# Kernel optimization log

Measured on AMD Instinct MI355X. Metric: run time of the kernel, lower is better.

The kernel has to match this reference:

```python
import jax, jax.numpy as jnp
import numpy as np

D_MODEL = 1024
D_STATE = 16
D_CONV = 4
EXPAND = 2
D_INNER = EXPAND * D_MODEL
DT_RANK = (D_MODEL + 15) // 16  # 64
EPS = 1e-5


def dwconv(x, w, b, pad):
    # x: (B, C, L), w: (C, 1, K), depthwise conv
    y = jax.lax.conv_general_dilated(x, w, (1,), [pad],
                                     dimension_numbers=('NCH', 'OIH', 'NCH'),
                                     feature_group_count=x.shape[1])
    return y + b[None, :, None]


def mamba(x, W_inproj, m_conv_w, m_conv_b, W_xproj, W_dt, b_dt, A_log, Dp, W_outproj):
    # x: (B, L, d_model)
    Bn, L, _ = x.shape
    xz = x @ W_inproj.T                       # (B, L, 2*d_inner)
    xi, z = jnp.split(xz, 2, axis=-1)
    # causal depthwise conv: pad (K-1, 0) == torch pad K-1 then slice [:L]
    xc = dwconv(jnp.swapaxes(xi, 1, 2), m_conv_w, m_conv_b, (D_CONV - 1, 0))
    u = jax.nn.silu(jnp.swapaxes(xc, 1, 2))   # (B, L, d_inner)
    x_dbl = u @ W_xproj.T                     # (B, L, dt_rank + 2*d_state)
    dt = x_dbl[..., :DT_RANK]
    Bm = x_dbl[..., DT_RANK:DT_RANK + D_STATE]
    Cm = x_dbl[..., DT_RANK + D_STATE:]
    dt = jax.nn.softplus(dt @ W_dt.T + b_dt)  # (B, L, d_inner)
    A = -jnp.exp(A_log)                       # (d_inner, d_state)

    def step(h, inp):
        dt_t, B_t, C_t, u_t = inp             # (B,di),(B,ds),(B,ds),(B,di)
        dA = jnp.exp(dt_t[..., None] * A)     # (B, di, ds)
        h = dA * h + dt_t[..., None] * B_t[:, None, :] * u_t[..., None]
        y = jnp.einsum('bds,bs->bd', h, C_t)
        return h, y

    tm = lambda a: jnp.swapaxes(a, 0, 1)      # time-major for scan
    h0 = jnp.zeros((Bn, D_INNER, D_STATE), x.dtype)
    _, ys = jax.lax.scan(step, h0, (tm(dt), tm(Bm), tm(Cm), tm(u)))
    y = jnp.swapaxes(ys, 0, 1) + u * Dp       # (B, L, d_inner)
    y = y * jax.nn.silu(z)
    return y @ W_outproj.T                    # (B, L, d_model)


def forward(x, ln_g, ln_b, W_in, b_in, conv_w, conv_b,
            W_inproj, m_conv_w, m_conv_b, W_xproj, W_dt, b_dt,
            A_log, Dp, W_outproj, W_out, b_out):
    h = jnp.swapaxes(x, 1, 2)                 # (B, L, d_model)
    mu = h.mean(-1, keepdims=True)
    var = ((h - mu) ** 2).mean(-1, keepdims=True)
    h = (h - mu) / jnp.sqrt(var + EPS) * ln_g + ln_b
    h = h @ W_in.T + b_in
    # outer depthwise conv: kernel 4, pad 2 each side -> length L+1 (faithful)
    h = dwconv(jnp.swapaxes(h, 1, 2), conv_w, conv_b, (D_CONV // 2, D_CONV // 2))
    h = jax.nn.silu(h)
    h = jnp.swapaxes(h, 1, 2)                 # (B, L+1, d_model)
    y = mamba(h, W_inproj, m_conv_w, m_conv_b, W_xproj, W_dt, b_dt, A_log, Dp, W_outproj)
    y = y @ W_out.T + b_out
    return jnp.swapaxes(y, 1, 2)              # (B, d_model, L+1)


def setup_inputs() -> dict:
    key = jax.random.key(0)
    ks = jax.random.split(key, 16)
    B, L = 2, 2048
    s = 0.02
    inp = {
        'x': jax.random.normal(ks[0], (B, D_MODEL, L), jnp.float32),
        'ln_g': jnp.ones((D_MODEL,), jnp.float32),
        'ln_b': jnp.zeros((D_MODEL,), jnp.float32),
        'W_in': jax.random.normal(ks[1], (D_MODEL, D_MODEL), jnp.float32) * s,
        'b_in': jnp.zeros((D_MODEL,), jnp.float32),
        'conv_w': jax.random.normal(ks[2], (D_MODEL, 1, D_CONV), jnp.float32) * 0.3,
        'conv_b': jnp.zeros((D_MODEL,), jnp.float32),
        'W_inproj': jax.random.normal(ks[3], (2 * D_INNER, D_MODEL), jnp.float32) * s,
        'm_conv_w': jax.random.normal(ks[4], (D_INNER, 1, D_CONV), jnp.float32) * 0.3,
        'm_conv_b': jnp.zeros((D_INNER,), jnp.float32),
        'W_xproj': jax.random.normal(ks[5], (DT_RANK + 2 * D_STATE, D_INNER), jnp.float32) * s,
        'W_dt': jax.random.normal(ks[6], (D_INNER, DT_RANK), jnp.float32) * (DT_RANK ** -0.5),
        'b_dt': jax.random.uniform(ks[7], (D_INNER,), jnp.float32, -4.6, -2.0),
        'A_log': jnp.log(jnp.tile(jnp.arange(1, D_STATE + 1, dtype=jnp.float32)[None, :], (D_INNER, 1))),
        'Dp': jnp.ones((D_INNER,), jnp.float32),
        'W_outproj': jax.random.normal(ks[8], (D_MODEL, D_INNER), jnp.float32) * s,
        'W_out': jax.random.normal(ks[9], (D_MODEL, D_MODEL), jnp.float32) * s,
        'b_out': jnp.zeros((D_MODEL,), jnp.float32),
    }
    return inp


def reference(x, ln_g, ln_b, W_in, b_in, conv_w, conv_b, W_inproj, m_conv_w, m_conv_b,
              W_xproj, W_dt, b_dt, A_log, Dp, W_outproj, W_out, b_out):
    return forward(x, ln_g, ln_b, W_in, b_in, conv_w, conv_b, W_inproj, m_conv_w,
                   m_conv_b, W_xproj, W_dt, b_dt, A_log, Dp, W_outproj, W_out, b_out)
```

## Files before the change

### kernel.cpp

```cpp
#include <hip/hip_runtime.h>
#include <hip/hip_bf16.h>

#define DMODEL 1024
#define DINNER 2048
#define DTRANK 64
#define NPROJ  96
#define BATCH  2
#define LIN    2048
#define LOUT   2049
#define MTOT0  4096
#define MTOT1  4098
#define TC     64
#define NCH    33

typedef __attribute__((ext_vector_type(8))) short short8;
typedef __attribute__((ext_vector_type(4))) float f32x4;

__device__ __forceinline__ float f_silu(float x)     { return x / (1.f + __expf(-x)); }
__device__ __forceinline__ float f_softplus(float x) { return (x > 20.f) ? x : log1pf(__expf(x)); }
__device__ __forceinline__ short f2b(float x)
{
    __hip_bfloat16 b = __float2bfloat16(x);
    return *reinterpret_cast<short*>(&b);
}
__device__ __forceinline__ float b2f(short s)
{
    return __uint_as_float(((unsigned)(unsigned short)s) << 16);
}
__device__ __forceinline__ void gload16(const void* g, void* l)
{
    __builtin_amdgcn_global_load_lds(
        (const __attribute__((address_space(1))) void*)g,
        (__attribute__((address_space(3))) void*)l,
        16, 0, 0);
}

__global__ void ln_stats_k(const float* __restrict__ x, float* __restrict__ mu, float* __restrict__ rs)
{
    int b  = blockIdx.y;
    int l0 = blockIdx.x * 64;
    int lc = threadIdx.x & 63;
    int q  = threadIdx.x >> 6;
    const float* xb = x + (size_t)b * DMODEL * LIN + (l0 + lc);
    float s = 0.f, ss = 0.f;
    for (int c = q * 256; c < q * 256 + 256; ++c) {
        float v = xb[(size_t)c * LIN];
        s += v; ss += v * v;
    }
    __shared__ float Ss[4][64];
    __shared__ float Sq[4][64];
    Ss[q][lc] = s; Sq[q][lc] = ss;
    __syncthreads();
    if (threadIdx.x < 64) {
        float st = Ss[0][lc] + Ss[1][lc] + Ss[2][lc] + Ss[3][lc];
        float sq = Sq[0][lc] + Sq[1][lc] + Sq[2][lc] + Sq[3][lc];
        float m = st * (1.f / DMODEL);
        float v = sq * (1.f / DMODEL) - m * m;
        mu[b * LIN + l0 + lc] = m;
        rs[b * LIN + l0 + lc] = 1.f / sqrtf(v + 1e-5f);
    }
}

__global__ void lnT_k(const float* __restrict__ x, const float* __restrict__ mu,
                      const float* __restrict__ rs, const float* __restrict__ g,
                      const float* __restrict__ be, short* __restrict__ h0T)
{
    __shared__ float T[32][33];
    int l0 = blockIdx.x * 32;
    int c0 = blockIdx.y * 32;
    int b  = blockIdx.z;
    int tx = threadIdx.x & 31, ty = threadIdx.x >> 5;
    const float* xb = x + ((size_t)b * DMODEL + c0) * LIN + l0;
#pragma unroll
    for (int i = 0; i < 4; i++) {
        int cl = ty + 8 * i;
        T[cl][tx] = xb[(size_t)cl * LIN + tx];
    }
    __syncthreads();
    int c = c0 + tx;
    float gg = g[c], bb = be[c];
#pragma unroll
    for (int i = 0; i < 4; i++) {
        int ll = ty + 8 * i;
        int m = b * LIN + l0 + ll;
        float v = (T[tx][ll] - mu[m]) * rs[m] * gg + bb;
        h0T[(size_t)m * DMODEL + c] = f2b(v);
    }
}

__global__ void wdtT_k(const float* __restrict__ W_dt, float* __restrict__ WdtT)
{
    __shared__ float T[32][33];
    int n0 = blockIdx.x * 32;
    int k0 = blockIdx.y * 32;
    int tx = threadIdx.x & 31, ty = threadIdx.x >> 5;
#pragma unroll
    for (int i = 0; i < 4; i++) {
        int r = ty + 8 * i;
        T[r][tx] = W_dt[(size_t)(n0 + r) * 64 + k0 + tx];
    }
    __syncthreads();
#pragma unroll
    for (int i = 0; i < 4; i++) {
        int r = ty + 8 * i;
        WdtT[(size_t)(k0 + r) * 2048 + n0 + tx] = T[tx][r];
    }
}

__global__ void cvt_all_k(const float* __restrict__ W_in, const float* __restrict__ W_inproj,
                          const float* __restrict__ W_xproj, const float* __restrict__ W_dt,
                          const float* __restrict__ W_outproj, const float* __restrict__ W_out,
                          short* __restrict__ Wib, short* __restrict__ Winpb,
                          short* __restrict__ Wxpb, short* __restrict__ Wdtb,
                          short* __restrict__ Wopb, short* __restrict__ Wob)
{
    int b = blockIdx.x;
    const float* s; short* d; int i;
    if      (b < 1024) { s = W_in;      d = Wib;   i = b; }
    else if (b < 5120) { s = W_inproj;  d = Winpb; i = b - 1024; }
    else if (b < 5312) { s = W_xproj;   d = Wxpb;  i = b - 5120; }
    else if (b < 5440) { s = W_dt;      d = Wdtb;  i = b - 5312; }
    else if (b < 7488) { s = W_outproj; d = Wopb;  i = b - 5440; }
    else               { s = W_out;     d = Wob;   i = b - 7488; }
    int idx = (i * 256 + threadIdx.x) * 4;
    float4 v = *(const float4*)(s + idx);
    d[idx + 0] = f2b(v.x); d[idx + 1] = f2b(v.y);
    d[idx + 2] = f2b(v.z); d[idx + 3] = f2b(v.w);
}

template<int EPI>
__global__ __launch_bounds__(256) void gemm_bf(
    const short* __restrict__ A, int lda,
    const short* __restrict__ W, int ldb,
    float* __restrict__ C, int ldc,
    short* __restrict__ Cb, int ldcb,
    int M, int N, int K,
    const float* __restrict__ bias)
{
    __shared__ short As[128 * 32];
    __shared__ short Bs[128 * 32];
    int tid  = threadIdx.x;
    int lane = tid & 63, wid = tid >> 6;
    int wr = wid >> 1, wc = wid & 1;
    int fr = lane & 15, kg = lane >> 4;
    int m0 = blockIdx.x * 128, n0 = blockIdx.y * 128;

    int scol  = (lane & 3) * 8;
    int srow0 = wid * 32 + (lane >> 2);
    int srow1 = srow0 + 16;
    const short* a0 = A + (size_t)(m0 + srow0) * lda + scol;
    const short* a1 = A + (size_t)(m0 + srow1) * lda + scol;
    const short* b0 = W + (size_t)(n0 + srow0) * ldb + scol;
    const short* b1 = W + (size_t)(n0 + srow1) * ldb + scol;
    char* asd0 = (char*)As + (wid * 2 + 0) * 1024;
    char* asd1 = (char*)As + (wid * 2 + 1) * 1024;
    char* bsd0 = (char*)Bs + (wid * 2 + 0) * 1024;
    char* bsd1 = (char*)Bs + (wid * 2 + 1) * 1024;

    f32x4 acc[4][4];
#pragma unroll
    for (int mi = 0; mi < 4; mi++)
#pragma unroll
        for (int ni = 0; ni < 4; ni++) acc[mi][ni] = (f32x4){0.f, 0.f, 0.f, 0.f};

    for (int k0 = 0; k0 < K; k0 += 32) {
        gload16(a0 + k0, asd0);
        gload16(a1 + k0, asd1);
        gload16(b0 + k0, bsd0);
        gload16(b1 + k0, bsd1);
        __syncthreads();

        short8 af[4], bf[4];
#pragma unroll
        for (int mi = 0; mi < 4; mi++)
            af[mi] = *(const short8*)&As[(wr * 64 + mi * 16 + fr) * 32 + kg * 8];
#pragma unroll
        for (int ni = 0; ni < 4; ni++)
            bf[ni] = *(const short8*)&Bs[(wc * 64 + ni * 16 + fr) * 32 + kg * 8];
#pragma unroll
        for (int mi = 0; mi < 4; mi++)
#pragma unroll
            for (int ni = 0; ni < 4; ni++)
                acc[mi][ni] = __builtin_amdgcn_mfma_f32_16x16x32_bf16(
                    af[mi], bf[ni], acc[mi][ni], 0, 0, 0);
        __syncthreads();
    }

#pragma unroll
    for (int ni = 0; ni < 4; ni++) {
        int n = n0 + wc * 64 + ni * 16 + fr;
        if (n >= N) continue;
        float bv = 0.f;
        if (EPI == 1) bv = bias[n];
#pragma unroll
        for (int mi = 0; mi < 4; mi++) {
#pragma unroll
            for (int r = 0; r < 4; r++) {
                int m = m0 + wr * 64 + mi * 16 + kg * 4 + r;
                if (m >= M) continue;
                float v = acc[mi][ni][r];
                if (EPI == 1) v += bv;
                if (EPI == 5) {
                    float vb = v + bias[m];
                    int bq = (n >= LOUT) ? 1 : 0;
                    int l  = n - bq * LOUT;
                    C[((size_t)bq * DMODEL + m) * LOUT + l] = vb;
                } else if (EPI == 4) {
                    Cb[(size_t)m * ldcb + n] = f2b(v);
                } else {
                    C[(size_t)m * ldc + n] = v;
                }
            }
        }
    }
}

__global__ __launch_bounds__(256) void dtfuse2_k(const float* __restrict__ xdbl,
                                                 const float* __restrict__ WdtT,
                                                 const float* __restrict__ b_dt,
                                                 float* __restrict__ dtout)
{
    int t  = threadIdx.x;
    int m0 = blockIdx.x * 8;
    __shared__ float dr[8][64];
    {
        int k = t & 63, r = t >> 6;
        int ma = m0 + r, mb = m0 + r + 4;
        dr[r][k]     = (ma < MTOT1) ? xdbl[(size_t)ma * NPROJ + k] : 0.f;
        dr[r + 4][k] = (mb < MTOT1) ? xdbl[(size_t)mb * NPROJ + k] : 0.f;
    }
    __syncthreads();

    int n0 = t * 4;
    f32x4 acc0[8], acc1[8];
#pragma unroll
    for (int mi = 0; mi < 8; mi++) {
        acc0[mi] = (f32x4){0.f, 0.f, 0.f, 0.f};
        acc1[mi] = (f32x4){0.f, 0.f, 0.f, 0.f};
    }

    for (int k = 0; k < 64; k += 4) {
        f32x4 w0[4], w1[4];
#pragma unroll
        for (int e = 0; e < 4; e++) {
            w0[e] = *(const f32x4*)&WdtT[(size_t)(k + e) * 2048 + n0];
            w1[e] = *(const f32x4*)&WdtT[(size_t)(k + e) * 2048 + n0 + 1024];
        }
#pragma unroll
        for (int mi = 0; mi < 8; mi++) {
            f32x4 d = *(const f32x4*)&dr[mi][k];
#pragma unroll
            for (int e = 0; e < 4; e++) {
                acc0[mi] += d[e] * w0[e];
                acc1[mi] += d[e] * w1[e];
            }
        }
    }

    f32x4 b0 = *(const f32x4*)&b_dt[n0];
    f32x4 b1 = *(const f32x4*)&b_dt[n0 + 1024];
#pragma unroll
    for (int mi = 0; mi < 8; mi++) {
        int m = m0 + mi;
        if (m >= MTOT1) continue;
        f32x4 v0, v1;
#pragma unroll
        for (int e = 0; e < 4; e++) {
            v0[e] = f_softplus(acc0[mi][e] + b0[e]);
            v1[e] = f_softplus(acc1[mi][e] + b1[e]);
        }
        *(f32x4*)&dtout[(size_t)m * DINNER + n0]        = v0;
        *(f32x4*)&dtout[(size_t)m * DINNER + n0 + 1024] = v1;
    }
}

__global__ void conv1_k(const float* __restrict__ h1, const float* __restrict__ cw,
                        const float* __restrict__ cb, short* __restrict__ h2b)
{
    int c = blockIdx.x * 256 + threadIdx.x;
    int m = blockIdx.y;
    int b = (m >= LOUT) ? 1 : 0;
    int l = m - b * LOUT;
    float4 wv = ((const float4*)cw)[c];
    const float* w = (const float*)&wv;
    float acc = cb[c];
#pragma unroll
    for (int k = 0; k < 4; k++) {
        int li = l - 2 + k;
        if (li >= 0 && li < LIN)
            acc += h1[((size_t)b * LIN + li) * DMODEL + c] * w[k];
    }
    h2b[(size_t)m * DMODEL + c] = f2b(f_silu(acc));
}

__global__ void conv2_k(const float* __restrict__ xz, const float* __restrict__ cw,
                        const float* __restrict__ cb, float* __restrict__ u,
                        short* __restrict__ ub)
{
    int d = blockIdx.x * 256 + threadIdx.x;
    int m = blockIdx.y;
    int b = (m >= LOUT) ? 1 : 0;
    int l = m - b * LOUT;
    float4 wv = ((const float4*)cw)[d];
    const float* w = (const float*)&wv;
    float acc = cb[d];
#pragma unroll
    for (int k = 0; k < 4; k++) {
        int li = l - 3 + k;
        if (li >= 0)
            acc += xz[((size_t)b * LOUT + li) * (2 * DINNER) + d] * w[k];
    }
    float s = f_silu(acc);
    u [(size_t)m * DINNER + d] = s;
    ub[(size_t)m * DINNER + d] = f2b(s);
}

__global__ void scan1_k(const float* __restrict__ dt, const float* __restrict__ u,
                        const float* __restrict__ xdbl, const float* __restrict__ A_log,
                        float* __restrict__ sP, float* __restrict__ sH)
{
    int d = blockIdx.x * 256 + threadIdx.x;
    int c = blockIdx.y;
    int b = blockIdx.z;
    int t0 = c * TC;
    int tlen = LOUT - t0; if (tlen > TC) tlen = TC;

    float Ad[16], h[16], P[16];
#pragma unroll
    for (int q = 0; q < 4; q++) {
        float4 av = ((const float4*)A_log)[d * 4 + q];
        Ad[q*4+0] = -__expf(av.x); Ad[q*4+1] = -__expf(av.y);
        Ad[q*4+2] = -__expf(av.z); Ad[q*4+3] = -__expf(av.w);
    }
#pragma unroll
    for (int s = 0; s < 16; s++) { h[s] = 0.f; P[s] = 1.f; }

    size_t row0 = (size_t)b * LOUT + t0;
    const float* dtp = dt + row0 * DINNER + d;
    const float* up  = u  + row0 * DINNER + d;
    const float* Bp  = xdbl + row0 * NPROJ + DTRANK;
    for (int t = 0; t < tlen; t++) {
        float dtt = dtp[(size_t)t * DINNER];
        float du  = dtt * up[(size_t)t * DINNER];
        const float* Bt = Bp + (size_t)t * NPROJ;
#pragma unroll
        for (int s = 0; s < 16; s++) {
            float a = __expf(dtt * Ad[s]);
            h[s] = a * h[s] + du * Bt[s];
            P[s] *= a;
        }
    }
    size_t base = ((size_t)(b * NCH + c) * 16) * DINNER + d;
#pragma unroll
    for (int s = 0; s < 16; s++) {
        sP[base + (size_t)s * DINNER] = P[s];
        sH[base + (size_t)s * DINNER] = h[s];
    }
}

__global__ void scan2_k(const float* __restrict__ sP, float* __restrict__ sH)
{
    int gid = blockIdx.x * 256 + threadIdx.x;
    int d = gid & (DINNER - 1);
    int s = (gid >> 11) & 15;
    int b = gid >> 15;
    size_t base = ((size_t)(b * NCH) * 16 + s) * DINNER + d;
    const size_t cstep = (size_t)16 * DINNER;
    float hrun = 0.f;
    for (int c = 0; c < NCH; c++) {
        size_t idx = base + (size_t)c * cstep;
        float Pv = sP[idx], hl = sH[idx];
        sH[idx] = hrun;
        hrun = Pv * hrun + hl;
    }
}

__global__ void scan3_k(const float* __restrict__ dt, const float* __restrict__ u,
                        const float* __restrict__ xdbl, const float* __restrict__ A_log,
                        const float* __restrict__ Dp, const float* __restrict__ xz,
                        const float* __restrict__ sH, short* __restrict__ ymb)
{
    int d = blockIdx.x * 256 + threadIdx.x;
    int c = blockIdx.y;
    int b = blockIdx.z;
    int t0 = c * TC;
    int tlen = LOUT - t0; if (tlen > TC) tlen = TC;

    float Ad[16], h[16];
#pragma unroll
    for (int q = 0; q < 4; q++) {
        float4 av = ((const float4*)A_log)[d * 4 + q];
        Ad[q*4+0] = -__expf(av.x); Ad[q*4+1] = -__expf(av.y);
        Ad[q*4+2] = -__expf(av.z); Ad[q*4+3] = -__expf(av.w);
    }
    size_t sbase = ((size_t)(b * NCH + c) * 16) * DINNER + d;
#pragma unroll
    for (int s = 0; s < 16; s++) h[s] = sH[sbase + (size_t)s * DINNER];

    float Dpd = Dp[d];
    size_t row0 = (size_t)b * LOUT + t0;
    const float* dtp = dt + row0 * DINNER + d;
    const float* up  = u  + row0 * DINNER + d;
    const float* Bp  = xdbl + row0 * NPROJ + DTRANK;
    const float* Cp  = Bp + 16;
    const float* zp  = xz + row0 * (2 * DINNER) + DINNER + d;
    short* yp = ymb + row0 * DINNER + d;
    for (int t = 0; t < tlen; t++) {
        float dtt = dtp[(size_t)t * DINNER];
        float ut  = up[(size_t)t * DINNER];
        float du  = dtt * ut;
        const float* Bt = Bp + (size_t)t * NPROJ;
        const float* Ct = Cp + (size_t)t * NPROJ;
        float y = 0.f;
#pragma unroll
        for (int s = 0; s < 16; s++) {
            float a = __expf(dtt * Ad[s]);
            h[s] = a * h[s] + du * Bt[s];
            y += h[s] * Ct[s];
        }
        float z = zp[(size_t)t * (2 * DINNER)];
        yp[(size_t)t * DINNER] = f2b((y + ut * Dpd) * f_silu(z));
    }
}

extern "C" void kernel_launch(void* const* d_in, const int* in_sizes, int n_in,
                              void* d_out, int out_size, void* d_ws, size_t ws_size,
                              hipStream_t stream)
{
    (void)in_sizes; (void)n_in; (void)out_size; (void)ws_size;
    const float* x        = (const float*)d_in[0];
    const float* ln_g     = (const float*)d_in[1];
    const float* ln_b     = (const float*)d_in[2];
    const float* W_in     = (const float*)d_in[3];
    const float* b_in     = (const float*)d_in[4];
    const float* conv_w   = (const float*)d_in[5];
    const float* conv_b   = (const float*)d_in[6];
    const float* W_inproj = (const float*)d_in[7];
    const float* m_conv_w = (const float*)d_in[8];
    const float* m_conv_b = (const float*)d_in[9];
    const float* W_xproj  = (const float*)d_in[10];
    const float* W_dt     = (const float*)d_in[11];
    const float* b_dt     = (const float*)d_in[12];
    const float* A_log    = (const float*)d_in[13];
    const float* Dp       = (const float*)d_in[14];
    const float* W_outproj= (const float*)d_in[15];
    const float* W_out    = (const float*)d_in[16];
    const float* b_out    = (const float*)d_in[17];
    float* out = (float*)d_out;

    float* F    = (float*)d_ws;
    float* mu   = F;
    float* rs   = F + 4096;
    float* h1   = F + 8192;
    float* xz   = h1 + (size_t)MTOT0 * DMODEL;
    float* uu   = xz + (size_t)MTOT1 * 2 * DINNER;
    float* xdbl = uu + (size_t)MTOT1 * DINNER;
    float* dt   = xdbl + (size_t)MTOT1 * NPROJ;
    float* sP   = dt + (size_t)MTOT1 * DINNER;
    float* sH   = sP + (size_t)BATCH * NCH * 16 * DINNER;
    float* WdtT = sH + (size_t)BATCH * NCH * 16 * DINNER;
    float* fend = WdtT + (size_t)DTRANK * DINNER;

    short* S     = (short*)fend;
    short* h0T   = S;
    short* h2b   = h0T + (size_t)MTOT0 * DMODEL;
    short* ub    = h2b + (size_t)MTOT1 * DMODEL;
    short* Wib   = ub  + (size_t)MTOT1 * DINNER;
    short* Winpb = Wib   + (size_t)DMODEL * DMODEL;
    short* Wxpb  = Winpb + (size_t)(2*DINNER) * DMODEL;
    short* Wdtb  = Wxpb  + (size_t)NPROJ * DINNER;
    short* Wopb  = Wdtb  + (size_t)DINNER * DTRANK;
    short* Wob   = Wopb  + (size_t)DMODEL * DINNER;
    short* ymb   = ub;
    short* o1b   = (short*)h1;

    cvt_all_k<<<8512, 256, 0, stream>>>(W_in, W_inproj, W_xproj, W_dt, W_outproj, W_out,
                                        Wib, Winpb, Wxpb, Wdtb, Wopb, Wob);
    wdtT_k<<<dim3(64, 2), 256, 0, stream>>>(W_dt, WdtT);
    ln_stats_k<<<dim3(32, 2), 256, 0, stream>>>(x, mu, rs);
    lnT_k<<<dim3(64, 32, 2), 256, 0, stream>>>(x, mu, rs, ln_g, ln_b, h0T);
    gemm_bf<1><<<dim3(32, 8), 256, 0, stream>>>(h0T, DMODEL, Wib, DMODEL,
        h1, DMODEL, nullptr, 0, MTOT0, DMODEL, DMODEL, b_in);
    conv1_k<<<dim3(4, MTOT1), 256, 0, stream>>>(h1, conv_w, conv_b, h2b);
    gemm_bf<0><<<dim3(33, 32), 256, 0, stream>>>(h2b, DMODEL, Winpb, DMODEL,
        xz, 2 * DINNER, nullptr, 0, MTOT1, 2 * DINNER, DMODEL, nullptr);
    conv2_k<<<dim3(8, MTOT1), 256, 0, stream>>>(xz, m_conv_w, m_conv_b, uu, ub);
    gemm_bf<0><<<dim3(33, 1), 256, 0, stream>>>(ub, DINNER, Wxpb, DINNER,
        xdbl, NPROJ, nullptr, 0, MTOT1, NPROJ, DINNER, nullptr);
    dtfuse2_k<<<513, 256, 0, stream>>>(xdbl, WdtT, b_dt, dt);
    scan1_k<<<dim3(8, NCH, 2), 256, 0, stream>>>(dt, uu, xdbl, A_log, sP, sH);
    scan2_k<<<dim3(256), 256, 0, stream>>>(sP, sH);
    scan3_k<<<dim3(8, NCH, 2), 256, 0, stream>>>(dt, uu, xdbl, A_log, Dp, xz, sH, ymb);
    gemm_bf<4><<<dim3(33, 8), 256, 0, stream>>>(ymb, DINNER, Wopb, DINNER,
        nullptr, 0, o1b, DMODEL, MTOT1, DMODEL, DINNER, nullptr);
    gemm_bf<5><<<dim3(8, 33), 256, 0, stream>>>(Wob, DMODEL, o1b, DMODEL,
        out, 0, nullptr, 0, DMODEL, MTOT1, DMODEL, b_out);
}
```

Baseline: 564.5 us.

## Stage GEMM epilogue through LDS, swizzle blocks across XCDs, halve scan chunk

The GEMM epilogue now writes accumulators into an LDS tile and stores coalesced 16-wide vector rows instead of scattered scalar stores. The block index is remapped with an XCD swizzle so that neighbouring tiles land on the same die's L2. The scan chunk length drops from 64 to 32, giving 65 chunks and more parallel blocks in the scan kernels. The unused W_dt bf16 conversion is removed. These trade extra LDS use and barriers in the epilogue, and larger scan carry buffers, for better store coalescing and cache locality.

```diff
diff --git a/kernel.cpp b/kernel.cpp
--- a/kernel.cpp
+++ b/kernel.cpp
@@ -10,8 +10,8 @@
 #define LOUT   2049
 #define MTOT0  4096
 #define MTOT1  4098
-#define TC     64
-#define NCH    33
+#define TC     32
+#define NCH    65
 
 typedef __attribute__((ext_vector_type(8))) short short8;
 typedef __attribute__((ext_vector_type(4))) float f32x4;
@@ -22,10 +22,6 @@
 {
     __hip_bfloat16 b = __float2bfloat16(x);
     return *reinterpret_cast<short*>(&b);
-}
-__device__ __forceinline__ float b2f(short s)
-{
-    return __uint_as_float(((unsigned)(unsigned short)s) << 16);
 }
 __device__ __forceinline__ void gload16(const void* g, void* l)
 {
@@ -33,6 +29,17 @@
         (const __attribute__((address_space(1))) void*)g,
         (__attribute__((address_space(3))) void*)l,
         16, 0, 0);
+}
+__device__ __forceinline__ void xcd_swizzle(int& bx, int& by)
+{
+    int nx = gridDim.x;
+    int nwg = nx * gridDim.y;
+    int f = blockIdx.x + blockIdx.y * nx;
+    int xcd = f & 7, i = f >> 3;
+    int q = nwg >> 3, r = nwg & 7;
+    int w = (xcd < r ? xcd * (q + 1) : r * (q + 1) + (xcd - r) * q) + i;
+    bx = w % nx;
+    by = w / nx;
 }
 
 __global__ void ln_stats_k(const float* __restrict__ x, float* __restrict__ mu, float* __restrict__ rs)
@@ -108,10 +115,10 @@
 }
 
 __global__ void cvt_all_k(const float* __restrict__ W_in, const float* __restrict__ W_inproj,
-                          const float* __restrict__ W_xproj, const float* __restrict__ W_dt,
+                          const float* __restrict__ W_xproj,
                           const float* __restrict__ W_outproj, const float* __restrict__ W_out,
                           short* __restrict__ Wib, short* __restrict__ Winpb,
-                          short* __restrict__ Wxpb, short* __restrict__ Wdtb,
+                          short* __restrict__ Wxpb,
                           short* __restrict__ Wopb, short* __restrict__ Wob)
 {
     int b = blockIdx.x;
@@ -119,9 +126,8 @@
     if      (b < 1024) { s = W_in;      d = Wib;   i = b; }
     else if (b < 5120) { s = W_inproj;  d = Winpb; i = b - 1024; }
     else if (b < 5312) { s = W_xproj;   d = Wxpb;  i = b - 5120; }
-    else if (b < 5440) { s = W_dt;      d = Wdtb;  i = b - 5312; }
-    else if (b < 7488) { s = W_outproj; d = Wopb;  i = b - 5440; }
-    else               { s = W_out;     d = Wob;   i = b - 7488; }
+    else if (b < 7360) { s = W_outproj; d = Wopb;  i = b - 5312; }
+    else               { s = W_out;     d = Wob;   i = b - 7360; }
     int idx = (i * 256 + threadIdx.x) * 4;
     float4 v = *(const float4*)(s + idx);
     d[idx + 0] = f2b(v.x); d[idx + 1] = f2b(v.y);
@@ -137,13 +143,17 @@
     int M, int N, int K,
     const float* __restrict__ bias)
 {
-    __shared__ short As[128 * 32];
-    __shared__ short Bs[128 * 32];
+    __shared__ char LDSall[16896];
+    short* As = (short*)LDSall;
+    short* Bs = (short*)(LDSall + 8192);
+
     int tid  = threadIdx.x;
     int lane = tid & 63, wid = tid >> 6;
     int wr = wid >> 1, wc = wid & 1;
     int fr = lane & 15, kg = lane >> 4;
-    int m0 = blockIdx.x * 128, n0 = blockIdx.y * 128;
+    int bx, by;
+    xcd_swizzle(bx, by);
+    int m0 = bx * 128, n0 = by * 128;
 
     int scol  = (lane & 3) * 8;
     int srow0 = wid * 32 + (lane >> 2);
@@ -152,10 +162,10 @@
     const short* a1 = A + (size_t)(m0 + srow1) * lda + scol;
     const short* b0 = W + (size_t)(n0 + srow0) * ldb + scol;
     const short* b1 = W + (size_t)(n0 + srow1) * ldb + scol;
-    char* asd0 = (char*)As + (wid * 2 + 0) * 1024;
-    char* asd1 = (char*)As + (wid * 2 + 1) * 1024;
-    char* bsd0 = (char*)Bs + (wid * 2 + 0) * 1024;
-    char* bsd1 = (char*)Bs + (wid * 2 + 1) * 1024;
+    char* asd0 = LDSall + (wid * 2 + 0) * 1024;
+    char* asd1 = LDSall + (wid * 2 + 1) * 1024;
+    char* bsd0 = LDSall + 8192 + (wid * 2 + 0) * 1024;
+    char* bsd1 = LDSall + 8192 + (wid * 2 + 1) * 1024;
 
     f32x4 acc[4][4];
 #pragma unroll
@@ -186,30 +196,54 @@
         __syncthreads();
     }
 
-#pragma unroll
-    for (int ni = 0; ni < 4; ni++) {
-        int n = n0 + wc * 64 + ni * 16 + fr;
-        if (n >= N) continue;
-        float bv = 0.f;
-        if (EPI == 1) bv = bias[n];
-#pragma unroll
-        for (int mi = 0; mi < 4; mi++) {
-#pragma unroll
-            for (int r = 0; r < 4; r++) {
-                int m = m0 + wr * 64 + mi * 16 + kg * 4 + r;
-                if (m >= M) continue;
-                float v = acc[mi][ni][r];
-                if (EPI == 1) v += bv;
-                if (EPI == 5) {
-                    float vb = v + bias[m];
-                    int bq = (n >= LOUT) ? 1 : 0;
-                    int l  = n - bq * LOUT;
-                    C[((size_t)bq * DMODEL + m) * LOUT + l] = vb;
-                } else if (EPI == 4) {
-                    Cb[(size_t)m * ldcb + n] = f2b(v);
-                } else {
-                    C[(size_t)m * ldc + n] = v;
+    float* ctile = (float*)LDSall;
+    int row = tid >> 3;
+    int cs  = (tid & 7) * 16;
+#pragma unroll
+    for (int p = 0; p < 4; p++) {
+        __syncthreads();
+#pragma unroll
+        for (int ni = 0; ni < 4; ni++)
+#pragma unroll
+            for (int r = 0; r < 4; r++)
+                ctile[(wr * 16 + kg * 4 + r) * 132 + wc * 64 + ni * 16 + fr] = acc[p][ni][r];
+        __syncthreads();
+        int mrow = m0 + ((row < 16) ? (p * 16 + row) : (64 + p * 16 + (row - 16)));
+        int n = n0 + cs;
+        if (mrow >= M || n >= N) continue;
+        const float* src = &ctile[row * 132 + cs];
+        if (EPI == 5) {
+            float bv = bias[mrow];
+            if (n + 15 < N && !(n < LOUT && n + 15 >= LOUT)) {
+                int bq = (n >= LOUT) ? 1 : 0;
+                float* dst = C + ((size_t)bq * DMODEL + mrow) * LOUT + (n - bq * LOUT);
+#pragma unroll
+                for (int e = 0; e < 4; e++) {
+                    f32x4 v = *(const f32x4*)(src + 4 * e);
+                    v += bv;
+                    *(f32x4*)(dst + 4 * e) = v;
                 }
+            } else {
+                for (int j = 0; j < 16; j++) {
+                    int nj = n + j;
+                    if (nj < N) {
+                        int bq = (nj >= LOUT) ? 1 : 0;
+                        C[((size_t)bq * DMODEL + mrow) * LOUT + (nj - bq * LOUT)] = src[j] + bv;
+                    }
+                }
+            }
+        } else if (EPI == 4) {
+            short8 o0, o1;
+#pragma unroll
+            for (int e = 0; e < 8; e++) { o0[e] = f2b(src[e]); o1[e] = f2b(src[8 + e]); }
+            *(short8*)&Cb[(size_t)mrow * ldcb + n]     = o0;
+            *(short8*)&Cb[(size_t)mrow * ldcb + n + 8] = o1;
+        } else {
+#pragma unroll
+            for (int e = 0; e < 4; e++) {
+                f32x4 v = *(const f32x4*)(src + 4 * e);
+                if (EPI == 1) v += *(const f32x4*)&bias[n + 4 * e];
+                *(f32x4*)&C[(size_t)mrow * ldc + n + 4 * e] = v;
             }
         }
     }
@@ -468,14 +502,13 @@
     short* Wib   = ub  + (size_t)MTOT1 * DINNER;
     short* Winpb = Wib   + (size_t)DMODEL * DMODEL;
     short* Wxpb  = Winpb + (size_t)(2*DINNER) * DMODEL;
-    short* Wdtb  = Wxpb  + (size_t)NPROJ * DINNER;
-    short* Wopb  = Wdtb  + (size_t)DINNER * DTRANK;
+    short* Wopb  = Wxpb  + (size_t)NPROJ * DINNER;
     short* Wob   = Wopb  + (size_t)DMODEL * DINNER;
     short* ymb   = ub;
     short* o1b   = (short*)h1;
 
-    cvt_all_k<<<8512, 256, 0, stream>>>(W_in, W_inproj, W_xproj, W_dt, W_outproj, W_out,
-                                        Wib, Winpb, Wxpb, Wdtb, Wopb, Wob);
+    cvt_all_k<<<8384, 256, 0, stream>>>(W_in, W_inproj, W_xproj, W_outproj, W_out,
+                                        Wib, Winpb, Wxpb, Wopb, Wob);
     wdtT_k<<<dim3(64, 2), 256, 0, stream>>>(W_dt, WdtT);
     ln_stats_k<<<dim3(32, 2), 256, 0, stream>>>(x, mu, rs);
     lnT_k<<<dim3(64, 32, 2), 256, 0, stream>>>(x, mu, rs, ln_g, ln_b, h0T);
```

New measurement: 631.6 us. 1.12x slower.
